# Kernel optimization log

Measured on AMD Instinct MI355X. Metric: run time of the kernel, lower is better.

Reference implementation:

```python
import jax, jax.numpy as jnp
import numpy as np

D, DFF, H = 1024, 4096, 16
B, S, L = 4, 4096, 512


def setup_inputs() -> dict:
    key = jax.random.key(0)
    ks = jax.random.split(key, 16)
    w = lambda k, shape: (jax.random.normal(k, shape, jnp.float32) * 0.02)
    return {
        "x": jax.random.normal(ks[0], (B, S, D), jnp.float32),
        "limited_time_offer": jax.random.normal(ks[1], (B, L, D), jnp.float32),
        "src_src_self_mask": jnp.ones((B, 1, 1, S), bool),
        "lto_src_cross_mask": jnp.ones((B, 1, 1, S), bool),
        "sa_wq": w(ks[2], (D, D)), "sa_wk": w(ks[3], (D, D)),
        "sa_wv": w(ks[4], (D, D)), "sa_wo": w(ks[5], (D, D)),
        "ca_wq": w(ks[6], (D, D)), "ca_wk": w(ks[7], (D, D)),
        "ca_wv": w(ks[8], (D, D)), "ca_wo": w(ks[9], (D, D)),
        "ff_w1": w(ks[10], (D, DFF)), "ff_b1": jnp.zeros((DFF,), jnp.float32),
        "ff_w2": w(ks[11], (DFF, D)), "ff_b2": jnp.zeros((D,), jnp.float32),
        "ln1_a": jnp.ones((D,), jnp.float32), "ln1_b": jnp.zeros((D,), jnp.float32),
        "ln2_a": jnp.ones((D,), jnp.float32), "ln2_b": jnp.zeros((D,), jnp.float32),
        "ln3_a": jnp.ones((D,), jnp.float32), "ln3_b": jnp.zeros((D,), jnp.float32),
    }


def _ln(x, alpha, bias, eps=1e-6):
    # torch: (x - mean) / (std + eps), std is UNBIASED (ddof=1)
    mean = x.mean(axis=-1, keepdims=True)
    std = jnp.sqrt(x.var(axis=-1, ddof=1, keepdims=True))
    return alpha * (x - mean) / (std + eps) + bias


def _mha_linear(q_in, k_in, v_in, wq, wk, wv, wo):
    Bq, Nq, d = q_in.shape
    dk = d // H
    def proj(t, w):
        t = t @ w  # [b, n, d]
        return t.reshape(t.shape[0], t.shape[1], H, dk).transpose(0, 2, 1, 3)  # bhnd
    Q = jax.nn.relu(proj(q_in, wq)) + 1e-6
    K = jax.nn.relu(proj(k_in, wk)) + 1e-6
    V = proj(v_in, wv)
    kv = jnp.einsum('bhnd,bhne->bhde', K, V)          # KV outer-product state
    qk = jnp.einsum('bhnd,bhde->bhne', Q, kv)         # [b, h, nq, dk]
    # faithful to torch einsum('bhnd,bhne->bhn', Q, K.sum(2, keepdim)):
    # broadcasts n and sums d and e independently
    norm = 1.0 / (Q.sum(-1) * K.sum((2, 3))[:, :, None] + 1e-6)  # [b, h, nq]
    out = (qk * norm[..., None]).transpose(0, 2, 1, 3).reshape(Bq, Nq, d)
    return out @ wo


def reference(x, limited_time_offer, src_src_self_mask, lto_src_cross_mask,
              sa_wq, sa_wk, sa_wv, sa_wo,
              ca_wq, ca_wk, ca_wv, ca_wo,
              ff_w1, ff_b1, ff_w2, ff_b2,
              ln1_a, ln1_b, ln2_a, ln2_b, ln3_a, ln3_b):
    # residual 0: self attention on x
    xn = _ln(x, ln1_a, ln1_b)
    x = x + _mha_linear(xn, xn, xn, sa_wq, sa_wk, sa_wv, sa_wo)
    # residual 1: cross attention, queries = normed lto, keys/values = updated x
    lton = _ln(limited_time_offer, ln2_a, ln2_b)
    lto = limited_time_offer + _mha_linear(lton, x, x, ca_wq, ca_wk, ca_wv, ca_wo)
    # residual 2: feed forward
    fn = _ln(lto, ln3_a, ln3_b)
    ff = jax.nn.relu(fn @ ff_w1 + ff_b1) @ ff_w2 + ff_b2
    return lto + ff
```

## Files before the change

### kernel.cpp

```cpp
#include <hip/hip_runtime.h>
#include <hip/hip_bf16.h>

#define BATCH 4
#define SEQ   4096
#define LSEQ  512
#define DMODEL 1024
#define DFF_  4096
#define NHEAD 16
#define DK_   64
#define NSPLIT 8
#define FFSK  8

typedef __attribute__((ext_vector_type(4))) float f32x4;
typedef __attribute__((ext_vector_type(8))) __bf16 bf16x8;
typedef __attribute__((ext_vector_type(8))) unsigned short ushort8v;
typedef unsigned short u16;

__device__ __forceinline__ u16 f2bf(float f) {
  union { float f; unsigned int u; } c; c.f = f;
  unsigned int u = c.u;
  u += 0x7fffu + ((u >> 16) & 1u);
  return (u16)(u >> 16);
}
__device__ __forceinline__ float bf2f(u16 h) {
  union { unsigned int u; float f; } c; c.u = ((unsigned int)h) << 16;
  return c.f;
}
__device__ __forceinline__ void gload16(const void* g, void* l) {
  __builtin_amdgcn_global_load_lds(
      (const __attribute__((address_space(1))) unsigned int*)g,
      (__attribute__((address_space(3))) unsigned int*)l, 16, 0, 0);
}

__global__ __launch_bounds__(256) void ln_kernel(
    const float* __restrict__ x, const float* __restrict__ alpha,
    const float* __restrict__ beta, u16* __restrict__ y)
{
  const int row = blockIdx.x;
  const int t = threadIdx.x;
  const float4 v = ((const float4*)(x + (size_t)row * DMODEL))[t];
  float s = v.x + v.y + v.z + v.w;
  float ss = v.x * v.x + v.y * v.y + v.z * v.z + v.w * v.w;
  for (int off = 32; off >= 1; off >>= 1) {
    s += __shfl_xor(s, off);
    ss += __shfl_xor(ss, off);
  }
  __shared__ float sbuf[4], ssbuf[4];
  int w = t >> 6;
  if ((t & 63) == 0) { sbuf[w] = s; ssbuf[w] = ss; }
  __syncthreads();
  s = sbuf[0] + sbuf[1] + sbuf[2] + sbuf[3];
  ss = ssbuf[0] + ssbuf[1] + ssbuf[2] + ssbuf[3];
  float mean = s * (1.f / DMODEL);
  float var = (ss - mean * mean * DMODEL) * (1.f / (DMODEL - 1));
  var = fmaxf(var, 0.f);
  float inv = 1.f / (sqrtf(var) + 1e-6f);
  const float4 a = ((const float4*)alpha)[t];
  const float4 bb = ((const float4*)beta)[t];
  ushort4 o;
  o.x = f2bf(a.x * (v.x - mean) * inv + bb.x);
  o.y = f2bf(a.y * (v.y - mean) * inv + bb.y);
  o.z = f2bf(a.z * (v.z - mean) * inv + bb.z);
  o.w = f2bf(a.w * (v.w - mean) * inv + bb.w);
  ((ushort4*)(y + (size_t)row * DMODEL))[t] = o;
}

__global__ __launch_bounds__(256) void wconv_t_kernel(
    const float* __restrict__ W, u16* __restrict__ Wt, int K, int N)
{
  __shared__ float tile[32][33];
  const int n0 = blockIdx.x * 32, k0 = blockIdx.y * 32;
  const int t = threadIdx.x;
  const int r = t >> 3, c4 = (t & 7) * 4;
  float4 v = *(const float4*)&W[(size_t)(k0 + r) * N + n0 + c4];
  tile[r][c4 + 0] = v.x; tile[r][c4 + 1] = v.y;
  tile[r][c4 + 2] = v.z; tile[r][c4 + 3] = v.w;
  __syncthreads();
  ushort4 o;
  o.x = f2bf(tile[c4 + 0][r]);
  o.y = f2bf(tile[c4 + 1][r]);
  o.z = f2bf(tile[c4 + 2][r]);
  o.w = f2bf(tile[c4 + 3][r]);
  *(ushort4*)&Wt[(size_t)(n0 + r) * K + k0 + c4] = o;
}

template <int ACT, bool BIAS, bool RESID, bool OUTBF, bool SPLITK>
__global__ __launch_bounds__(512, 2) void gemm256(
    const u16* __restrict__ A, const u16* __restrict__ Bt,
    const float* __restrict__ bias, const float* __restrict__ R,
    void* __restrict__ Cout, int M, int N, int K, int lda, int ldb)
{
  __shared__ u16 sh[2][2][256 * 64];
  const int t = threadIdx.x;
  const int wid = t >> 6, lane = t & 63;
  const int wr = wid >> 2, wc = wid & 3;
  const int fr = lane & 15, fg = lane >> 4;

  if (SPLITK) {
    const int kp = blockIdx.y;
    A += (size_t)kp * K;
    Bt += (size_t)kp * K;
  }

  int bid = blockIdx.x;
  {
    const int nwg = gridDim.x;
    int q = nwg >> 3, rmd = nwg & 7;
    int xcd = bid & 7, idx = bid >> 3;
    bid = (xcd < rmd ? xcd * (q + 1) : rmd * (q + 1) + (xcd - rmd) * q) + idx;
  }
  const int nxb = N >> 8;
  const int m0 = (bid / nxb) * 256, n0 = (bid % nxb) * 256;

  auto stageA = [&](int buf, int h, int kt) {
#pragma unroll
    for (int j = 0; j < 2; ++j) {
      int idx = j * 512 + t;
      int r = idx >> 3;
      int gc = ((idx & 7) * 16) ^ ((r & 7) << 4);
      const char* src = (const char*)(A + (size_t)(m0 + h * 128 + r) * lda + kt * 64) + gc;
      char* dst = (char*)&sh[buf][0][0] + h * 16384 + j * 8192 + wid * 1024;
      gload16(src, dst);
    }
  };
  auto stageB = [&](int buf, int h, int kt) {
#pragma unroll
    for (int j = 0; j < 2; ++j) {
      int idx = j * 512 + t;
      int r = idx >> 3;
      int gc = ((idx & 7) * 16) ^ ((r & 7) << 4);
      const char* src = (const char*)(Bt + (size_t)(n0 + h * 128 + r) * ldb + kt * 64) + gc;
      char* dst = (char*)&sh[buf][1][0] + h * 16384 + j * 8192 + wid * 1024;
      gload16(src, dst);
    }
  };
  auto rdA = [&](int buf, int mi, int kk) -> bf16x8 {
    int r = wr * 128 + mi * 16 + fr;
    int c = (kk * 64 + fg * 16) ^ ((r & 7) << 4);
    return *(const bf16x8*)((const char*)&sh[buf][0][0] + r * 128 + c);
  };
  auto rdB = [&](int buf, int ni, int kk) -> bf16x8 {
    int r = wc * 64 + ni * 16 + fr;
    int c = (kk * 64 + fg * 16) ^ ((r & 7) << 4);
    return *(const bf16x8*)((const char*)&sh[buf][1][0] + r * 128 + c);
  };

  f32x4 acc[8][4] = {};
  bf16x8 bfrag[4][2];

#define PHASE(BUF, Q, STAGE_STMT, VCNT) do {                                          \
    bf16x8 a00 = rdA(BUF, (Q)*2, 0),     a01 = rdA(BUF, (Q)*2, 1);                     \
    bf16x8 a10 = rdA(BUF, (Q)*2 + 1, 0), a11 = rdA(BUF, (Q)*2 + 1, 1);                 \
    if ((Q) == 0) {                                                                    \
      _Pragma("unroll") for (int ni = 0; ni < 4; ++ni) {                               \
        bfrag[ni][0] = rdB(BUF, ni, 0); bfrag[ni][1] = rdB(BUF, ni, 1); } }            \
    STAGE_STMT;                                                                        \
    __builtin_amdgcn_s_barrier();                                                      \
    asm volatile("s_waitcnt lgkmcnt(0)" ::: "memory");                                 \
    __builtin_amdgcn_s_setprio(1);                                                     \
    _Pragma("unroll") for (int ni = 0; ni < 4; ++ni) {                                 \
      acc[(Q)*2][ni]     = __builtin_amdgcn_mfma_f32_16x16x32_bf16(a00, bfrag[ni][0], acc[(Q)*2][ni], 0, 0, 0);     \
      acc[(Q)*2][ni]     = __builtin_amdgcn_mfma_f32_16x16x32_bf16(a01, bfrag[ni][1], acc[(Q)*2][ni], 0, 0, 0);     \
      acc[(Q)*2 + 1][ni] = __builtin_amdgcn_mfma_f32_16x16x32_bf16(a10, bfrag[ni][0], acc[(Q)*2 + 1][ni], 0, 0, 0); \
      acc[(Q)*2 + 1][ni] = __builtin_amdgcn_mfma_f32_16x16x32_bf16(a11, bfrag[ni][1], acc[(Q)*2 + 1][ni], 0, 0, 0); } \
    __builtin_amdgcn_s_setprio(0);                                                     \
    if ((VCNT) == 4) { asm volatile("s_waitcnt vmcnt(4)" ::: "memory"); }              \
    else if ((VCNT) == 0) { asm volatile("s_waitcnt vmcnt(0)" ::: "memory"); }         \
    __builtin_amdgcn_s_barrier();                                                      \
  } while (0)

  stageA(0, 0, 0); stageA(0, 1, 0);
  stageB(0, 0, 0); stageB(0, 1, 0);
  stageB(1, 0, 1); stageB(1, 1, 1);
  asm volatile("s_waitcnt vmcnt(4)" ::: "memory");
  __builtin_amdgcn_s_barrier();

  const int NIT = K >> 7;
  for (int i = 0; i < NIT - 1; ++i) {
    const int t1 = 2 * i + 1, s0 = 2 * i + 2, s1 = 2 * i + 3;
    PHASE(0, 0, stageA(1, 0, t1), -1);
    PHASE(0, 1, stageA(1, 1, t1), -1);
    PHASE(0, 2, stageB(0, 0, s0), -1);
    PHASE(0, 3, stageB(0, 1, s0), 4);
    PHASE(1, 0, stageA(0, 0, s0), -1);
    PHASE(1, 1, stageA(0, 1, s0), -1);
    PHASE(1, 2, stageB(1, 0, s1), -1);
    PHASE(1, 3, stageB(1, 1, s1), 4);
  }
  {
    const int t1 = 2 * (NIT - 1) + 1;
    PHASE(0, 0, stageA(1, 0, t1), -1);
    PHASE(0, 1, stageA(1, 1, t1), -1);
    PHASE(0, 2, ((void)0), -1);
    PHASE(0, 3, ((void)0), 0);
    PHASE(1, 0, ((void)0), -1);
    PHASE(1, 1, ((void)0), -1);
    PHASE(1, 2, ((void)0), -1);
    PHASE(1, 3, ((void)0), -1);
  }
#undef PHASE

  float* Cf = (float*)Cout;
  if (SPLITK) Cf += (size_t)blockIdx.y * M * N;
  u16* Cb = (u16*)Cout;
#pragma unroll
  for (int mi = 0; mi < 8; ++mi)
#pragma unroll
    for (int ni = 0; ni < 4; ++ni)
#pragma unroll
      for (int r = 0; r < 4; ++r) {
        int row = m0 + wr * 128 + mi * 16 + fg * 4 + r;
        int col = n0 + wc * 64 + ni * 16 + fr;
        float v = acc[mi][ni][r];
        if (BIAS) v += bias[col];
        if (ACT == 1) v = fmaxf(v, 0.f);
        if (ACT == 2) v = fmaxf(v, 0.f) + 1e-6f;
        if (RESID) v += R[(size_t)row * N + col];
        if (OUTBF) Cb[(size_t)row * N + col] = f2bf(v);
        else       Cf[(size_t)row * N + col] = v;
      }
}

__global__ __launch_bounds__(256) void ffred_kernel(
    const float* __restrict__ part, const float* __restrict__ bias,
    const float* __restrict__ R, float* __restrict__ out)
{
  const int idx = blockIdx.x * 256 + threadIdx.x;
  const int c4 = idx & 255;
  float4 s = ((const float4*)R)[idx];
  const float4 bv = ((const float4*)bias)[c4];
  s.x += bv.x; s.y += bv.y; s.z += bv.z; s.w += bv.w;
#pragma unroll
  for (int p = 0; p < FFSK; ++p) {
    float4 v = ((const float4*)part)[(size_t)p * 524288 + idx];
    s.x += v.x; s.y += v.y; s.z += v.z; s.w += v.w;
  }
  ((float4*)out)[idx] = s;
}

__global__ __launch_bounds__(256) void ffred_h_kernel(
    const float* __restrict__ part, const float* __restrict__ bias,
    u16* __restrict__ outb)
{
  const size_t idx = (size_t)blockIdx.x * 256 + threadIdx.x;
  const int c4 = idx & 1023;
  const float4 bv = ((const float4*)bias)[c4];
  const float4 p0 = ((const float4*)part)[idx];
  const float4 p1 = ((const float4*)part)[idx + 2097152];
  ushort4 o;
  o.x = f2bf(fmaxf(p0.x + p1.x + bv.x, 0.f));
  o.y = f2bf(fmaxf(p0.y + p1.y + bv.y, 0.f));
  o.z = f2bf(fmaxf(p0.z + p1.z + bv.z, 0.f));
  o.w = f2bf(fmaxf(p0.w + p1.w + bv.w, 0.f));
  ((ushort4*)outb)[idx] = o;
}

template <int ACT, bool BIAS, bool RESID, bool OUTBF>
__global__ __launch_bounds__(256) void gemm_bf16(
    const u16* __restrict__ A, const u16* __restrict__ Bt,
    const float* __restrict__ bias, const float* __restrict__ R,
    void* __restrict__ Cout, int M, int N, int K)
{
  __shared__ u16 As[2][128 * 32];
  __shared__ u16 Bs[2][128 * 32];
  const int t = threadIdx.x;
  const int m0 = blockIdx.y * 128, n0 = blockIdx.x * 128;
  const int lane = t & 63, wid = t >> 6;
  const int wm = (wid >> 1) * 64, wn = (wid & 1) * 64;
  const int fr = lane & 15, fg = lane >> 4;

  const int srow = t >> 2;
  const int scol = (t & 3) * 8;
  const u16* aptr = A + (size_t)(m0 + srow) * K + scol;
  const u16* bptr = Bt + (size_t)(n0 + srow) * K + scol;
  const size_t rstep = (size_t)64 * K;

  f32x4 acc[4][4] = {};

  auto stage = [&](int c, int k0) {
    gload16(aptr + k0,         &As[c][wid * 512]);
    gload16(aptr + k0 + rstep, &As[c][2048 + wid * 512]);
    gload16(bptr + k0,         &Bs[c][wid * 512]);
    gload16(bptr + k0 + rstep, &Bs[c][2048 + wid * 512]);
  };
  auto compute = [&](int c) {
    bf16x8 af[4], bfr[4];
#pragma unroll
    for (int mi = 0; mi < 4; ++mi)
      af[mi] = *(const bf16x8*)&As[c][(wm + mi * 16 + fr) * 32 + fg * 8];
#pragma unroll
    for (int ni = 0; ni < 4; ++ni)
      bfr[ni] = *(const bf16x8*)&Bs[c][(wn + ni * 16 + fr) * 32 + fg * 8];
#pragma unroll
    for (int mi = 0; mi < 4; ++mi)
#pragma unroll
      for (int ni = 0; ni < 4; ++ni)
        acc[mi][ni] = __builtin_amdgcn_mfma_f32_16x16x32_bf16(af[mi], bfr[ni], acc[mi][ni], 0, 0, 0);
  };

  const int NT = K >> 5;
  stage(0, 0);
  asm volatile("s_waitcnt vmcnt(0)" ::: "memory");
  __builtin_amdgcn_s_barrier();
  int cur = 0;
  for (int kt = 0; kt < NT - 1; ++kt) {
    stage(cur ^ 1, (kt + 1) * 32);
    compute(cur);
    asm volatile("s_waitcnt vmcnt(0)" ::: "memory");
    __builtin_amdgcn_s_barrier();
    cur ^= 1;
  }
  compute(cur);

  float* Cf = (float*)Cout;
  u16* Cb = (u16*)Cout;
#pragma unroll
  for (int mi = 0; mi < 4; ++mi)
#pragma unroll
    for (int ni = 0; ni < 4; ++ni)
#pragma unroll
      for (int r = 0; r < 4; ++r) {
        int row = m0 + wm + mi * 16 + fg * 4 + r;
        int col = n0 + wn + ni * 16 + fr;
        float v = acc[mi][ni][r];
        if (BIAS) v += bias[col];
        if (ACT == 1) v = fmaxf(v, 0.f);
        if (ACT == 2) v = fmaxf(v, 0.f) + 1e-6f;
        if (RESID) v += R[(size_t)row * N + col];
        if (OUTBF) Cb[(size_t)row * N + col] = f2bf(v);
        else       Cf[(size_t)row * N + col] = v;
      }
}

__global__ __launch_bounds__(256) void kv_mfma_kernel(
    const u16* __restrict__ Kp, const u16* __restrict__ Vp,
    float* __restrict__ kvpart, float* __restrict__ kpart, int Ntok)
{
  const int h = blockIdx.x, b = blockIdx.y, sp = blockIdx.z;
  const int rows = Ntok / NSPLIT;
  const int nbeg = sp * rows;
  const u16* Kb = Kp + ((size_t)b * Ntok + nbeg) * DMODEL + h * DK_;
  const u16* Vb = Vp + ((size_t)b * Ntok + nbeg) * DMODEL + h * DK_;
  __shared__ u16 Kt[64 * 64];
  __shared__ u16 Vt[64 * 64];
  const int t = threadIdx.x;
  const int lane = t & 63, wid = t >> 6;
  const int fr = lane & 15, fg = lane >> 4;
  const int lrow = t >> 2;
  const int lc0 = (t & 3) * 16;

  f32x4 acc[4] = {};
  float kp = 0.f;

  ushort8v ck[2], cv[2];
  {
    const u16* kr = Kb + (size_t)lrow * DMODEL + lc0;
    const u16* vr = Vb + (size_t)lrow * DMODEL + lc0;
    ck[0] = *(const ushort8v*)kr; ck[1] = *(const ushort8v*)(kr + 8);
    cv[0] = *(const ushort8v*)vr; cv[1] = *(const ushort8v*)(vr + 8);
  }
  for (int c = 0; c < rows; c += 64) {
#pragma unroll
    for (int i = 0; i < 2; ++i)
#pragma unroll
      for (int j = 0; j < 8; ++j) kp += bf2f(ck[i][j]);
    __syncthreads();
#pragma unroll
    for (int i = 0; i < 2; ++i)
#pragma unroll
      for (int j = 0; j < 8; ++j) {
        int d = lc0 + i * 8 + j;
        int byteoff = (d * 128 + lrow * 2) ^ ((d & 7) << 4);
        *(u16*)((char*)Kt + byteoff) = ck[i][j];
        *(u16*)((char*)Vt + byteoff) = cv[i][j];
      }
    __syncthreads();
    if (c + 64 < rows) {
      const u16* kr = Kb + (size_t)(c + 64 + lrow) * DMODEL + lc0;
      const u16* vr = Vb + (size_t)(c + 64 + lrow) * DMODEL + lc0;
      ck[0] = *(const ushort8v*)kr; ck[1] = *(const ushort8v*)(kr + 8);
      cv[0] = *(const ushort8v*)vr; cv[1] = *(const ushort8v*)(vr + 8);
    }
#pragma unroll
    for (int ks = 0; ks < 2; ++ks) {
      bf16x8 bv;
      {
        int e = wid * 16 + fr;
        int byteoff = (e * 128 + (ks * 32 + fg * 8) * 2) ^ ((e & 7) << 4);
        bv = *(const bf16x8*)((const char*)Vt + byteoff);
      }
#pragma unroll
      for (int mi = 0; mi < 4; ++mi) {
        int d = mi * 16 + fr;
        int byteoff = (d * 128 + (ks * 32 + fg * 8) * 2) ^ ((d & 7) << 4);
        bf16x8 av = *(const bf16x8*)((const char*)Kt + byteoff);
        acc[mi] = __builtin_amdgcn_mfma_f32_16x16x32_bf16(av, bv, acc[mi], 0, 0, 0);
      }
    }
  }
  float* outp = kvpart + (((size_t)(b * NHEAD + h)) * NSPLIT + sp) * (DK_ * DK_);
#pragma unroll
  for (int mi = 0; mi < 4; ++mi)
#pragma unroll
    for (int r = 0; r < 4; ++r)
      outp[(mi * 16 + fg * 4 + r) * DK_ + wid * 16 + fr] = acc[mi][r];
  for (int off = 32; off >= 1; off >>= 1) kp += __shfl_xor(kp, off);
  __shared__ float kr4[4];
  if (lane == 0) kr4[wid] = kp;
  __syncthreads();
  if (t == 0) kpart[(b * NHEAD + h) * NSPLIT + sp] = kr4[0] + kr4[1] + kr4[2] + kr4[3];
}

__global__ __launch_bounds__(256) void kv_reduce_kernel(
    const float* __restrict__ kvpart, const float* __restrict__ kpart,
    u16* __restrict__ kvT, float* __restrict__ ksum)
{
  const int bh = blockIdx.x;
  const int t = threadIdx.x;
  for (int i = t; i < DK_ * DK_; i += 256) {
    int d = i >> 6, e = i & 63;
    float s = 0.f;
#pragma unroll
    for (int p = 0; p < NSPLIT; ++p)
      s += kvpart[((size_t)bh * NSPLIT + p) * (DK_ * DK_) + i];
    kvT[(size_t)bh * (DK_ * DK_) + e * DK_ + d] = f2bf(s);
  }
  if (t == 0) {
    float s = 0.f;
    for (int p = 0; p < NSPLIT; ++p) s += kpart[bh * NSPLIT + p];
    ksum[bh] = s;
  }
}

__global__ __launch_bounds__(256) void qk_mfma_kernel(
    const u16* __restrict__ Qp, const u16* __restrict__ kvT,
    const float* __restrict__ ksum, u16* __restrict__ AO, int Ntok)
{
  const int h = blockIdx.y, b = blockIdx.z;
  const int n0 = blockIdx.x * 128;
  const int t = threadIdx.x;
  const int lane = t & 63, wid = t >> 6;
  const int fr = lane & 15, fg = lane >> 4;

  __shared__ u16 Qs[128 * 64];
  __shared__ u16 KVs[64 * 64];
  __shared__ float qsl[128];

  auto swz = [](int byte, int row) { return byte ^ ((row & 7) << 4); };

  const u16* Qbase = Qp + ((size_t)b * Ntok + n0) * DMODEL + h * DK_;
#pragma unroll
  for (int j = 0; j < 4; ++j) {
    int id = t + 256 * j;
    int r = id >> 3, cseg = id & 7;
    ushort8v v = *(const ushort8v*)(Qbase + (size_t)r * DMODEL + cseg * 8);
    *(ushort8v*)((char*)Qs + swz(r * 128 + cseg * 16, r)) = v;
  }
  const u16* Kbase = kvT + ((size_t)(b * NHEAD + h)) * (DK_ * DK_);
#pragma unroll
  for (int j = 0; j < 2; ++j) {
    int id = t + 256 * j;
    int r = id >> 3, cseg = id & 7;
    ushort8v v = *(const ushort8v*)(Kbase + r * DK_ + cseg * 8);
    *(ushort8v*)((char*)KVs + swz(r * 128 + cseg * 16, r)) = v;
  }
  __syncthreads();

  {
    int row = t >> 1, part = t & 1;
    float s = 0.f;
#pragma unroll
    for (int j = 0; j < 4; ++j) {
      bf16x8 v = *(const bf16x8*)((char*)Qs + swz(row * 128 + (part * 4 + j) * 16, row));
#pragma unroll
      for (int i = 0; i < 8; ++i) s += (float)v[i];
    }
    s += __shfl_xor(s, 1);
    if (part == 0) qsl[row] = s;
  }

  const int wm = wid * 32;
  f32x4 acc[2][4] = {};
#pragma unroll
  for (int kk = 0; kk < 2; ++kk) {
    bf16x8 af[2], bfv[4];
#pragma unroll
    for (int mi = 0; mi < 2; ++mi) {
      int row = wm + mi * 16 + fr;
      af[mi] = *(const bf16x8*)((char*)Qs + swz(row * 128 + kk * 64 + fg * 16, row));
    }
#pragma unroll
    for (int ni = 0; ni < 4; ++ni) {
      int row = ni * 16 + fr;
      bfv[ni] = *(const bf16x8*)((char*)KVs + swz(row * 128 + kk * 64 + fg * 16, row));
    }
#pragma unroll
    for (int mi = 0; mi < 2; ++mi)
#pragma unroll
      for (int ni = 0; ni < 4; ++ni)
        acc[mi][ni] = __builtin_amdgcn_mfma_f32_16x16x32_bf16(af[mi], bfv[ni], acc[mi][ni], 0, 0, 0);
  }
  __syncthreads();

  const float ks = ksum[b * NHEAD + h];
  u16* AObase = AO + ((size_t)b * Ntok + n0) * DMODEL + h * DK_;
#pragma unroll
  for (int mi = 0; mi < 2; ++mi)
#pragma unroll
    for (int ni = 0; ni < 4; ++ni)
#pragma unroll
      for (int r = 0; r < 4; ++r) {
        int row = wm + mi * 16 + fg * 4 + r;
        int col = ni * 16 + fr;
        float rn = 1.f / (qsl[row] * ks + 1e-6f);
        AObase[(size_t)row * DMODEL + col] = f2bf(acc[mi][ni][r] * rn);
      }
}

extern "C" void kernel_launch(void* const* d_in, const int* in_sizes, int n_in,
                              void* d_out, int out_size, void* d_ws, size_t ws_size,
                              hipStream_t stream) {
  const float* x     = (const float*)d_in[0];
  const float* lto   = (const float*)d_in[1];
  const float* sa_wq = (const float*)d_in[4];
  const float* sa_wk = (const float*)d_in[5];
  const float* sa_wv = (const float*)d_in[6];
  const float* sa_wo = (const float*)d_in[7];
  const float* ca_wq = (const float*)d_in[8];
  const float* ca_wk = (const float*)d_in[9];
  const float* ca_wv = (const float*)d_in[10];
  const float* ca_wo = (const float*)d_in[11];
  const float* ff_w1 = (const float*)d_in[12];
  const float* ff_b1 = (const float*)d_in[13];
  const float* ff_w2 = (const float*)d_in[14];
  const float* ff_b2 = (const float*)d_in[15];
  const float* ln1_a = (const float*)d_in[16];
  const float* ln1_b = (const float*)d_in[17];
  const float* ln2_a = (const float*)d_in[18];
  const float* ln2_b = (const float*)d_in[19];
  const float* ln3_a = (const float*)d_in[20];
  const float* ln3_b = (const float*)d_in[21];
  float* out = (float*)d_out;

  char* wsb = (char*)d_ws;
  auto take = [&](size_t bytes) {
    char* p = wsb;
    wsb += (bytes + 255) & ~(size_t)255;
    return (void*)p;
  };
  u16* SAQT = (u16*)take(2097152);
  u16* SAKT = (u16*)take(2097152);
  u16* SAVT = (u16*)take(2097152);
  u16* SAOT = (u16*)take(2097152);
  u16* CQT  = (u16*)take(2097152);
  u16* CKT  = (u16*)take(2097152);
  u16* CVT  = (u16*)take(2097152);
  u16* COT  = (u16*)take(2097152);
  u16* FW1T = (u16*)take(8388608);
  u16* FW2T = (u16*)take(8388608);
  u16* R1 = (u16*)take(33554432);
  u16* R2 = (u16*)take(33554432);
  u16* R3 = (u16*)take(33554432);
  u16* S1 = (u16*)take(4194304);
  u16* S2 = (u16*)take(4194304);
  u16* S3 = (u16*)take(4194304);
  float* LTO1   = (float*)take(8388608);
  float* KVPART = (float*)take(8388608);
  u16*   KVT    = (u16*)take(1048576);
  float* KPART  = (float*)take(2048);
  float* KSUM   = (float*)take(256);
  float* FFPART = (float*)take((size_t)FFSK * 2048 * 1024 * 4);

  const int STOK = BATCH * SEQ;
  const int LTOK = BATCH * LSEQ;
  dim3 blk(256);
  dim3 blk512(512);
  dim3 gbig(STOK / 256 * (DMODEL / 256));

  wconv_t_kernel<<<dim3(32, 32), blk, 0, stream>>>(sa_wq, SAQT, 1024, 1024);
  wconv_t_kernel<<<dim3(32, 32), blk, 0, stream>>>(sa_wk, SAKT, 1024, 1024);
  wconv_t_kernel<<<dim3(32, 32), blk, 0, stream>>>(sa_wv, SAVT, 1024, 1024);
  wconv_t_kernel<<<dim3(32, 32), blk, 0, stream>>>(sa_wo, SAOT, 1024, 1024);
  wconv_t_kernel<<<dim3(32, 32), blk, 0, stream>>>(ca_wq, CQT, 1024, 1024);
  wconv_t_kernel<<<dim3(32, 32), blk, 0, stream>>>(ca_wk, CKT, 1024, 1024);
  wconv_t_kernel<<<dim3(32, 32), blk, 0, stream>>>(ca_wv, CVT, 1024, 1024);
  wconv_t_kernel<<<dim3(32, 32), blk, 0, stream>>>(ca_wo, COT, 1024, 1024);
  wconv_t_kernel<<<dim3(128, 32), blk, 0, stream>>>(ff_w1, FW1T, 1024, 4096);
  wconv_t_kernel<<<dim3(32, 128), blk, 0, stream>>>(ff_w2, FW2T, 4096, 1024);

  ln_kernel<<<STOK, blk, 0, stream>>>(x, ln1_a, ln1_b, R1);
  gemm256<2, false, false, true, false><<<gbig, blk512, 0, stream>>>(R1, SAKT, nullptr, nullptr, R2, STOK, 1024, 1024, 1024, 1024);
  gemm256<0, false, false, true, false><<<gbig, blk512, 0, stream>>>(R1, SAVT, nullptr, nullptr, R3, STOK, 1024, 1024, 1024, 1024);
  kv_mfma_kernel<<<dim3(NHEAD, BATCH, NSPLIT), blk, 0, stream>>>(R2, R3, KVPART, KPART, SEQ);
  kv_reduce_kernel<<<64, blk, 0, stream>>>(KVPART, KPART, KVT, KSUM);
  gemm256<2, false, false, true, false><<<gbig, blk512, 0, stream>>>(R1, SAQT, nullptr, nullptr, R2, STOK, 1024, 1024, 1024, 1024);
  qk_mfma_kernel<<<dim3(SEQ / 128, NHEAD, BATCH), blk, 0, stream>>>(R2, KVT, KSUM, R1, SEQ);
  gemm256<0, false, true, true, false><<<gbig, blk512, 0, stream>>>(R1, SAOT, nullptr, x, R3, STOK, 1024, 1024, 1024, 1024);

  ln_kernel<<<LTOK, blk, 0, stream>>>(lto, ln2_a, ln2_b, S1);
  gemm_bf16<2, false, false, true><<<dim3(8, 16), blk, 0, stream>>>(S1, CQT, nullptr, nullptr, S2, LTOK, 1024, 1024);
  gemm256<2, false, false, true, false><<<gbig, blk512, 0, stream>>>(R3, CKT, nullptr, nullptr, R2, STOK, 1024, 1024, 1024, 1024);
  gemm256<0, false, false, true, false><<<gbig, blk512, 0, stream>>>(R3, CVT, nullptr, nullptr, R1, STOK, 1024, 1024, 1024, 1024);
  kv_mfma_kernel<<<dim3(NHEAD, BATCH, NSPLIT), blk, 0, stream>>>(R2, R1, KVPART, KPART, SEQ);
  kv_reduce_kernel<<<64, blk, 0, stream>>>(KVPART, KPART, KVT, KSUM);
  qk_mfma_kernel<<<dim3(LSEQ / 128, NHEAD, BATCH), blk, 0, stream>>>(S2, KVT, KSUM, S3, LSEQ);
  gemm_bf16<0, false, true, false><<<dim3(8, 16), blk, 0, stream>>>(S3, COT, nullptr, lto, LTO1, LTOK, 1024, 1024);

  ln_kernel<<<LTOK, blk, 0, stream>>>(LTO1, ln3_a, ln3_b, S1);
  gemm256<0, false, false, false, true><<<dim3(128, 2), blk512, 0, stream>>>(S1, FW1T, nullptr, nullptr, FFPART, LTOK, 4096, 512, 1024, 1024);
  ffred_h_kernel<<<8192, blk, 0, stream>>>(FFPART, ff_b1, R2);
  gemm256<0, false, false, false, true><<<dim3(32, FFSK), blk512, 0, stream>>>(R2, FW2T, nullptr, nullptr, FFPART, LTOK, 1024, 512, 4096, 4096);
  ffred_kernel<<<2048, blk, 0, stream>>>(FFPART, ff_b2, LTO1, out);
}
```

Measured before the change: 510.7 us.

## Fuse Q/K/V projections into one wide GEMM with per-segment ReLU epilogue

Concatenates the transposed K, V and Q weights so the self-attention projections run as a single GEMM with N=3072, and the cross-attention K and V as one GEMM with N=2048. A new epilogue mode applies relu+eps only to the K and Q column segments, and the kv and qk kernels take a row stride to read the interleaved output. This removes separate launches and re-reading of the normalized activation, in exchange for a larger workspace buffer that is also reused for the FFN partial sums.

Result: faster. 495.7 us (-2.9%).

```diff
diff --git a/kernel.cpp b/kernel.cpp
--- a/kernel.cpp
+++ b/kernel.cpp
@@ -203,6 +203,7 @@
   float* Cf = (float*)Cout;
   if (SPLITK) Cf += (size_t)blockIdx.y * M * N;
   u16* Cb = (u16*)Cout;
+  const bool segRelu = (ACT == 3) ? ((n0 >> 10) != 1) : false;
 #pragma unroll
   for (int mi = 0; mi < 8; ++mi)
 #pragma unroll
@@ -215,6 +216,7 @@
         if (BIAS) v += bias[col];
         if (ACT == 1) v = fmaxf(v, 0.f);
         if (ACT == 2) v = fmaxf(v, 0.f) + 1e-6f;
+        if (ACT == 3 && segRelu) v = fmaxf(v, 0.f) + 1e-6f;
         if (RESID) v += R[(size_t)row * N + col];
         if (OUTBF) Cb[(size_t)row * N + col] = f2bf(v);
         else       Cf[(size_t)row * N + col] = v;
@@ -333,14 +335,14 @@
 }
 
 __global__ __launch_bounds__(256) void kv_mfma_kernel(
-    const u16* __restrict__ Kp, const u16* __restrict__ Vp,
-    float* __restrict__ kvpart, float* __restrict__ kpart, int Ntok)
+    const u16* __restrict__ KV, float* __restrict__ kvpart,
+    float* __restrict__ kpart, int Ntok, int ld)
 {
   const int h = blockIdx.x, b = blockIdx.y, sp = blockIdx.z;
   const int rows = Ntok / NSPLIT;
   const int nbeg = sp * rows;
-  const u16* Kb = Kp + ((size_t)b * Ntok + nbeg) * DMODEL + h * DK_;
-  const u16* Vb = Vp + ((size_t)b * Ntok + nbeg) * DMODEL + h * DK_;
+  const u16* Kb = KV + ((size_t)b * Ntok + nbeg) * ld + h * DK_;
+  const u16* Vb = Kb + 1024;
   __shared__ u16 Kt[64 * 64];
   __shared__ u16 Vt[64 * 64];
   const int t = threadIdx.x;
@@ -354,8 +356,8 @@
 
   ushort8v ck[2], cv[2];
   {
-    const u16* kr = Kb + (size_t)lrow * DMODEL + lc0;
-    const u16* vr = Vb + (size_t)lrow * DMODEL + lc0;
+    const u16* kr = Kb + (size_t)lrow * ld + lc0;
+    const u16* vr = Vb + (size_t)lrow * ld + lc0;
     ck[0] = *(const ushort8v*)kr; ck[1] = *(const ushort8v*)(kr + 8);
     cv[0] = *(const ushort8v*)vr; cv[1] = *(const ushort8v*)(vr + 8);
   }
@@ -376,8 +378,8 @@
       }
     __syncthreads();
     if (c + 64 < rows) {
-      const u16* kr = Kb + (size_t)(c + 64 + lrow) * DMODEL + lc0;
-      const u16* vr = Vb + (size_t)(c + 64 + lrow) * DMODEL + lc0;
+      const u16* kr = Kb + (size_t)(c + 64 + lrow) * ld + lc0;
+      const u16* vr = Vb + (size_t)(c + 64 + lrow) * ld + lc0;
       ck[0] = *(const ushort8v*)kr; ck[1] = *(const ushort8v*)(kr + 8);
       cv[0] = *(const ushort8v*)vr; cv[1] = *(const ushort8v*)(vr + 8);
     }
@@ -434,7 +436,7 @@
 
 __global__ __launch_bounds__(256) void qk_mfma_kernel(
     const u16* __restrict__ Qp, const u16* __restrict__ kvT,
-    const float* __restrict__ ksum, u16* __restrict__ AO, int Ntok)
+    const float* __restrict__ ksum, u16* __restrict__ AO, int Ntok, int ldq)
 {
   const int h = blockIdx.y, b = blockIdx.z;
   const int n0 = blockIdx.x * 128;
@@ -448,12 +450,12 @@
 
   auto swz = [](int byte, int row) { return byte ^ ((row & 7) << 4); };
 
-  const u16* Qbase = Qp + ((size_t)b * Ntok + n0) * DMODEL + h * DK_;
+  const u16* Qbase = Qp + ((size_t)b * Ntok + n0) * ldq + h * DK_;
 #pragma unroll
   for (int j = 0; j < 4; ++j) {
     int id = t + 256 * j;
     int r = id >> 3, cseg = id & 7;
-    ushort8v v = *(const ushort8v*)(Qbase + (size_t)r * DMODEL + cseg * 8);
+    ushort8v v = *(const ushort8v*)(Qbase + (size_t)r * ldq + cseg * 8);
     *(ushort8v*)((char*)Qs + swz(r * 128 + cseg * 16, r)) = v;
   }
   const u16* Kbase = kvT + ((size_t)(b * NHEAD + h)) * (DK_ * DK_);
@@ -548,19 +550,16 @@
     wsb += (bytes + 255) & ~(size_t)255;
     return (void*)p;
   };
-  u16* SAQT = (u16*)take(2097152);
-  u16* SAKT = (u16*)take(2097152);
-  u16* SAVT = (u16*)take(2097152);
+  u16* WKVQ = (u16*)take(6291456);
+  u16* WCKV = (u16*)take(4194304);
   u16* SAOT = (u16*)take(2097152);
   u16* CQT  = (u16*)take(2097152);
-  u16* CKT  = (u16*)take(2097152);
-  u16* CVT  = (u16*)take(2097152);
   u16* COT  = (u16*)take(2097152);
   u16* FW1T = (u16*)take(8388608);
   u16* FW2T = (u16*)take(8388608);
-  u16* R1 = (u16*)take(33554432);
-  u16* R2 = (u16*)take(33554432);
-  u16* R3 = (u16*)take(33554432);
+  u16* R1   = (u16*)take(33554432);
+  u16* KVQ  = (u16*)take(100663296);
+  u16* R3   = (u16*)take(33554432);
   u16* S1 = (u16*)take(4194304);
   u16* S2 = (u16*)take(4194304);
   u16* S3 = (u16*)take(4194304);
@@ -569,46 +568,47 @@
   u16*   KVT    = (u16*)take(1048576);
   float* KPART  = (float*)take(2048);
   float* KSUM   = (float*)take(256);
-  float* FFPART = (float*)take((size_t)FFSK * 2048 * 1024 * 4);
+  float* FFPART = (float*)KVQ;
 
   const int STOK = BATCH * SEQ;
   const int LTOK = BATCH * LSEQ;
   dim3 blk(256);
   dim3 blk512(512);
-  dim3 gbig(STOK / 256 * (DMODEL / 256));
-
-  wconv_t_kernel<<<dim3(32, 32), blk, 0, stream>>>(sa_wq, SAQT, 1024, 1024);
-  wconv_t_kernel<<<dim3(32, 32), blk, 0, stream>>>(sa_wk, SAKT, 1024, 1024);
-  wconv_t_kernel<<<dim3(32, 32), blk, 0, stream>>>(sa_wv, SAVT, 1024, 1024);
+
+  wconv_t_kernel<<<dim3(32, 32), blk, 0, stream>>>(sa_wk, WKVQ,           1024, 1024);
+  wconv_t_kernel<<<dim3(32, 32), blk, 0, stream>>>(sa_wv, WKVQ + 1048576, 1024, 1024);
+  wconv_t_kernel<<<dim3(32, 32), blk, 0, stream>>>(sa_wq, WKVQ + 2097152, 1024, 1024);
+  wconv_t_kernel<<<dim3(32, 32), blk, 0, stream>>>(ca_wk, WCKV,           1024, 1024);
+  wconv_t_kernel<<<dim3(32, 32), blk, 0, stream>>>(ca_wv, WCKV + 1048576, 1024, 1024);
   wconv_t_kernel<<<dim3(32, 32), blk, 0, stream>>>(sa_wo, SAOT, 1024, 1024);
   wconv_t_kernel<<<dim3(32, 32), blk, 0, stream>>>(ca_wq, CQT, 1024, 1024);
-  wconv_t_kernel<<<dim3(32, 32), blk, 0, stream>>>(ca_wk, CKT, 1024, 1024);
-  wconv_t_kernel<<<dim3(32, 32), blk, 0, stream>>>(ca_wv, CVT, 1024, 1024);
   wconv_t_kernel<<<dim3(32, 32), blk, 0, stream>>>(ca_wo, COT, 1024, 1024);
   wconv_t_kernel<<<dim3(128, 32), blk, 0, stream>>>(ff_w1, FW1T, 1024, 4096);
   wconv_t_kernel<<<dim3(32, 128), blk, 0, stream>>>(ff_w2, FW2T, 4096, 1024);
 
   ln_kernel<<<STOK, blk, 0, stream>>>(x, ln1_a, ln1_b, R1);
-  gemm256<2, false, false, true, false><<<gbig, blk512, 0, stream>>>(R1, SAKT, nullptr, nullptr, R2, STOK, 1024, 1024, 1024, 1024);
-  gemm256<0, false, false, true, false><<<gbig, blk512, 0, stream>>>(R1, SAVT, nullptr, nullptr, R3, STOK, 1024, 1024, 1024, 1024);
-  kv_mfma_kernel<<<dim3(NHEAD, BATCH, NSPLIT), blk, 0, stream>>>(R2, R3, KVPART, KPART, SEQ);
+  gemm256<3, false, false, true, false><<<dim3(64 * 12), blk512, 0, stream>>>(
+      R1, WKVQ, nullptr, nullptr, KVQ, STOK, 3072, 1024, 1024, 1024);
+  kv_mfma_kernel<<<dim3(NHEAD, BATCH, NSPLIT), blk, 0, stream>>>(KVQ, KVPART, KPART, SEQ, 3072);
   kv_reduce_kernel<<<64, blk, 0, stream>>>(KVPART, KPART, KVT, KSUM);
-  gemm256<2, false, false, true, false><<<gbig, blk512, 0, stream>>>(R1, SAQT, nullptr, nullptr, R2, STOK, 1024, 1024, 1024, 1024);
-  qk_mfma_kernel<<<dim3(SEQ / 128, NHEAD, BATCH), blk, 0, stream>>>(R2, KVT, KSUM, R1, SEQ);
-  gemm256<0, false, true, true, false><<<gbig, blk512, 0, stream>>>(R1, SAOT, nullptr, x, R3, STOK, 1024, 1024, 1024, 1024);
+  qk_mfma_kernel<<<dim3(SEQ / 128, NHEAD, BATCH), blk, 0, stream>>>(KVQ + 2048, KVT, KSUM, R1, SEQ, 3072);
+  gemm256<0, false, true, true, false><<<dim3(64 * 4), blk512, 0, stream>>>(
+      R1, SAOT, nullptr, x, R3, STOK, 1024, 1024, 1024, 1024);
 
   ln_kernel<<<LTOK, blk, 0, stream>>>(lto, ln2_a, ln2_b, S1);
   gemm_bf16<2, false, false, true><<<dim3(8, 16), blk, 0, stream>>>(S1, CQT, nullptr, nullptr, S2, LTOK, 1024, 1024);
-  gemm256<2, false, false, true, false><<<gbig, blk512, 0, stream>>>(R3, CKT, nullptr, nullptr, R2, STOK, 1024, 1024, 1024, 1024);
-  gemm256<0, false, false, true, false><<<gbig, blk512, 0, stream>>>(R3, CVT, nullptr, nullptr, R1, STOK, 1024, 1024, 1024, 1024);
-  kv_mfma_kernel<<<dim3(NHEAD, BATCH, NSPLIT), blk, 0, stream>>>(R2, R1, KVPART, KPART, SEQ);
+  gemm256<3, false, false, true, false><<<dim3(64 * 8), blk512, 0, stream>>>(
+      R3, WCKV, nullptr, nullptr, KVQ, STOK, 2048, 1024, 1024, 1024);
+  kv_mfma_kernel<<<dim3(NHEAD, BATCH, NSPLIT), blk, 0, stream>>>(KVQ, KVPART, KPART, SEQ, 2048);
   kv_reduce_kernel<<<64, blk, 0, stream>>>(KVPART, KPART, KVT, KSUM);
-  qk_mfma_kernel<<<dim3(LSEQ / 128, NHEAD, BATCH), blk, 0, stream>>>(S2, KVT, KSUM, S3, LSEQ);
+  qk_mfma_kernel<<<dim3(LSEQ / 128, NHEAD, BATCH), blk, 0, stream>>>(S2, KVT, KSUM, S3, LSEQ, 1024);
   gemm_bf16<0, false, true, false><<<dim3(8, 16), blk, 0, stream>>>(S3, COT, nullptr, lto, LTO1, LTOK, 1024, 1024);
 
   ln_kernel<<<LTOK, blk, 0, stream>>>(LTO1, ln3_a, ln3_b, S1);
-  gemm256<0, false, false, false, true><<<dim3(128, 2), blk512, 0, stream>>>(S1, FW1T, nullptr, nullptr, FFPART, LTOK, 4096, 512, 1024, 1024);
-  ffred_h_kernel<<<8192, blk, 0, stream>>>(FFPART, ff_b1, R2);
-  gemm256<0, false, false, false, true><<<dim3(32, FFSK), blk512, 0, stream>>>(R2, FW2T, nullptr, nullptr, FFPART, LTOK, 1024, 512, 4096, 4096);
+  gemm256<0, false, false, false, true><<<dim3(128, 2), blk512, 0, stream>>>(
+      S1, FW1T, nullptr, nullptr, FFPART, LTOK, 4096, 512, 1024, 1024);
+  ffred_h_kernel<<<8192, blk, 0, stream>>>(FFPART, ff_b1, R3);
+  gemm256<0, false, false, false, true><<<dim3(32, FFSK), blk512, 0, stream>>>(
+      R3, FW2T, nullptr, nullptr, FFPART, LTOK, 1024, 512, 4096, 4096);
   ffred_kernel<<<2048, blk, 0, stream>>>(FFPART, ff_b2, LTO1, out);
 }
```
